# Performance work log

Measured on AMD Instinct MI355X. Metric: run time of the kernel, lower is better.

The kernel has to match this reference:

```python
import jax, jax.numpy as jnp
import numpy as np

B, DIN, DOUT = 16, 64, 64
P1_, P2_, P3_ = 64, 32, 16
BN_EPS = 1e-5


def setup_inputs() -> dict:
    key = jax.random.key(0)
    ks = jax.random.split(key, 8)
    A = jax.random.normal(ks[0], (B, DIN, P1_, P2_, P3_), dtype=jnp.float32)
    ini_p = float(np.sqrt(3.0 / DOUT / DIN))
    ini_qk = float(np.sqrt(1.0 / DOUT / DIN))
    def uni(k, s):
        return jax.random.uniform(k, (DOUT, DIN), dtype=jnp.float32, minval=-s, maxval=s)
    return {
        "A": A,
        "P1": uni(ks[1], ini_p),
        "P2": uni(ks[2], ini_p),
        "P3": uni(ks[3], ini_p),
        "P4": uni(ks[4], ini_p),
        "q": uni(ks[5], ini_qk),
        "k": uni(ks[6], ini_qk),
        "gamma": jnp.ones((DOUT,), jnp.float32),
        "beta": jnp.zeros((DOUT,), jnp.float32),
        "permutation_size1": P1_,
        "permutation_size2": P2_,
        "permutation_size3": P3_,
        "BATCH_SIZE": B,
    }


def reference(A, P1, P2, P3, P4, q, k, gamma, beta,
              permutation_size1, permutation_size2, permutation_size3, BATCH_SIZE):
    b = BATCH_SIZE
    dout = P1.shape[0]
    p1, p2, p3 = permutation_size1, permutation_size2, permutation_size3
    # branch 1: full per-element channel mix  [B, dout, p1, p2, p3]
    A1 = jnp.einsum('oi,bixyz->boxyz', P1, A)
    # branch 2: mean over p3, project, broadcast over p3
    A2 = jnp.einsum('oi,bixy->boxy', P2, A.mean(-1))[..., None]
    # branch 3: mean over p2, project, broadcast over p2
    A3 = jnp.einsum('oi,bixz->boxz', P3, A.mean(-2))[:, :, :, None, :]
    # attention over p1 with flattened (p2*p3) as the contraction axis
    Q = jnp.einsum('oi,bixyz->boxyz', q, A).reshape(b, dout, p1, p2 * p3)
    K = jnp.einsum('oi,bixyz->boxyz', k, A).reshape(b, dout, p1, p2 * p3)
    Alpha = jnp.einsum('bcxm,bcym->bcxy', Q, K)  # [B, dout, p1, p1]
    Alpha_norm = jnp.abs(Alpha) / jnp.linalg.norm(Alpha, axis=3, keepdims=True)
    V = jnp.einsum('oi,bixyz->boxyz', P4, A).reshape(b, dout, p1, p2 * p3)
    Y = jnp.einsum('bcxy,bcym->bcxm', Alpha_norm, V).reshape(b, dout, p1, p2, p3)
    out = A1 + 0.1 * A2 + 0.1 * A3 + 0.1 * Y
    out = jax.nn.relu(out)
    # BatchNorm3d (training-mode batch statistics, biased variance)
    mean = out.mean(axis=(0, 2, 3, 4), keepdims=True)
    var = out.var(axis=(0, 2, 3, 4), keepdims=True)
    out = (out - mean) * jax.lax.rsqrt(var + BN_EPS)
    out = out * gamma[None, :, None, None, None] + beta[None, :, None, None, None]
    return out
```

## Files before the change

### kernel.cpp

```cpp
#include <hip/hip_runtime.h>

typedef __attribute__((ext_vector_type(8))) short short8;
typedef __attribute__((ext_vector_type(4))) float f32x4;
typedef __attribute__((ext_vector_type(8))) unsigned short u16x8;
typedef __attribute__((ext_vector_type(4))) unsigned short u16x4;
typedef __attribute__((ext_vector_type(4))) unsigned int u32x4;
typedef unsigned short u16;

#define DEVINL __device__ __forceinline__

DEVINL u16 f2bf(float f) {
  unsigned u = __builtin_bit_cast(unsigned, f);
  unsigned r = (u + 0x7fffu + ((u >> 16) & 1u)) >> 16;
  return (u16)r;
}
DEVINL float bf2f(u16 h) {
  unsigned u = ((unsigned)h) << 16;
  return __builtin_bit_cast(float, u);
}
DEVINL unsigned pk2(float a, float b) {
  return (unsigned)f2bf(a) | ((unsigned)f2bf(b) << 16);
}
DEVINL int swzc(int row, int chunk) { return chunk ^ ((row ^ (row >> 3)) & 7); }
DEVINL int tile_byte(int row, int chunk) { return row * 128 + swzc(row, chunk) * 16; }

__global__ void kw_convert(const float* __restrict__ P1, const float* __restrict__ q,
                           const float* __restrict__ k, const float* __restrict__ P4,
                           const float* __restrict__ P2, const float* __restrict__ P3,
                           u16* __restrict__ Wbf) {
  int t = threadIdx.x;
  const float* srcs[6] = {P1, q, k, P4, P2, P3};
  for (int w = 0; w < 6; ++w)
    for (int e = t; e < 4096; e += 256) Wbf[w * 4096 + e] = f2bf(srcs[w][e]);
}

__global__ __launch_bounds__(512) void k_projA(
    const float* __restrict__ A, const u16* __restrict__ Wbf, u16* __restrict__ A1,
    u16* __restrict__ Q, u16* __restrict__ Km, u16* __restrict__ V,
    float* __restrict__ A2g, float* __restrict__ m2p, int g0) {
  __shared__ __align__(16) u16 tile[256 * 64];
  __shared__ __align__(16) u16 meanT[16 * 64];
  const int t = threadIdx.x;
  const int w = t >> 6, l = t & 63;
  const int lr = l & 15, lh = l >> 4;
  const int T = blockIdx.x, bg = blockIdx.y;
  const int x = T >> 1, h = T & 1;
  const long bglob = g0 + bg;

  const int m = w & 3, sh = w >> 2;
  const u16* wb = Wbf + m * 4096;
  short8 wf[4][2];
#pragma unroll
  for (int ot = 0; ot < 4; ++ot)
#pragma unroll
    for (int ks = 0; ks < 2; ++ks)
      wf[ot][ks] = *(const short8*)(wb + (ot * 16 + lr) * 64 + ks * 32 + lh * 8);
  u16* outp = (m == 0) ? A1 : (m == 1) ? Q : (m == 2) ? Km : V;
  outp += (long)bg * 64 * 32768;
  const int odd = lh & 1;
  const int p8 = (lh >> 1) * 8;

  {
    const int s4 = t & 31, i4 = t >> 5;
    const float* ap =
        A + (bglob * 64 + i4 * 4) * 32768 + (long)x * 512 + h * 256 + s4 * 4;
#pragma unroll
    for (int si = 0; si < 2; ++si) {
      f32x4 v0 = *(const f32x4*)(ap + si * 128);
      f32x4 v1 = *(const f32x4*)(ap + si * 128 + 32768);
      f32x4 v2 = *(const f32x4*)(ap + si * 128 + 65536);
      f32x4 v3 = *(const f32x4*)(ap + si * 128 + 98304);
#pragma unroll
      for (int e = 0; e < 4; ++e) {
        int s = si * 128 + s4 * 4 + e;
        u16x4 pk = {f2bf(v0[e]), f2bf(v1[e]), f2bf(v2[e]), f2bf(v3[e])};
        *(u16x4*)((char*)tile + tile_byte(s, i4 >> 1) + (i4 & 1) * 8) = pk;
      }
    }
  }
  __syncthreads();

  {
    const int ic = t & 7, zq = (t >> 3) & 3, y16 = t >> 5;
    float acc[8] = {0, 0, 0, 0, 0, 0, 0, 0};
#pragma unroll
    for (int zz = 0; zz < 4; ++zz) {
      int row = y16 * 16 + zq * 4 + zz;
      u16x8 v = *(const u16x8*)((const char*)tile + tile_byte(row, ic));
#pragma unroll
      for (int e = 0; e < 8; ++e) acc[e] += bf2f(v[e]);
    }
#pragma unroll
    for (int e = 0; e < 8; ++e) {
      acc[e] += __shfl_xor(acc[e], 8);
      acc[e] += __shfl_xor(acc[e], 16);
    }
    if (zq == 0) {
      u16x8 pk;
#pragma unroll
      for (int e = 0; e < 8; ++e) pk[e] = f2bf(acc[e] * (1.0f / 16.0f));
      *(u16x8*)((char*)meanT + tile_byte(y16, ic)) = pk;
    }
  }
  {
    const int ic = t & 7, yg = (t >> 3) & 3, z = t >> 5;
    float acc[8] = {0, 0, 0, 0, 0, 0, 0, 0};
#pragma unroll
    for (int yy = 0; yy < 4; ++yy) {
      int row = (yg * 4 + yy) * 16 + z;
      u16x8 v = *(const u16x8*)((const char*)tile + tile_byte(row, ic));
#pragma unroll
      for (int e = 0; e < 8; ++e) acc[e] += bf2f(v[e]);
    }
#pragma unroll
    for (int e = 0; e < 8; ++e) {
      acc[e] += __shfl_xor(acc[e], 8);
      acc[e] += __shfl_xor(acc[e], 16);
    }
    if (yg == 0) {
      float* mp = m2p + (((long)bg * 64 + x) * 2 + h) * 1024 + z * 64 + ic * 8;
      *(f32x4*)(mp) = (f32x4){acc[0], acc[1], acc[2], acc[3]};
      *(f32x4*)(mp + 4) = (f32x4){acc[4], acc[5], acc[6], acc[7]};
    }
  }

  for (int stp = 0; stp < 4; ++stp) {
    const int srowE = sh * 128 + stp * 32 + lr;
    const int srowO = srowE + 16;
    short8 aE0 = *(const short8*)((const char*)tile + tile_byte(srowE, lh));
    short8 aE1 = *(const short8*)((const char*)tile + tile_byte(srowE, 4 + lh));
    short8 aO0 = *(const short8*)((const char*)tile + tile_byte(srowO, lh));
    short8 aO1 = *(const short8*)((const char*)tile + tile_byte(srowO, 4 + lh));
    const int sbase = x * 512 + h * 256 + sh * 128 + stp * 32 + odd * 16 + p8;
#pragma unroll
    for (int ot = 0; ot < 4; ++ot) {
      f32x4 accE = {0.0f, 0.0f, 0.0f, 0.0f}, accO = {0.0f, 0.0f, 0.0f, 0.0f};
      accE = __builtin_amdgcn_mfma_f32_16x16x32_bf16(aE0, wf[ot][0], accE, 0, 0, 0);
      accE = __builtin_amdgcn_mfma_f32_16x16x32_bf16(aE1, wf[ot][1], accE, 0, 0, 0);
      accO = __builtin_amdgcn_mfma_f32_16x16x32_bf16(aO0, wf[ot][0], accO, 0, 0, 0);
      accO = __builtin_amdgcn_mfma_f32_16x16x32_bf16(aO1, wf[ot][1], accO, 0, 0, 0);
      unsigned pE0 = pk2(accE[0], accE[1]), pE1 = pk2(accE[2], accE[3]);
      unsigned pO0 = pk2(accO[0], accO[1]), pO1 = pk2(accO[2], accO[3]);
      unsigned rE0 = __shfl_xor((int)pE0, 16), rE1 = __shfl_xor((int)pE1, 16);
      unsigned rO0 = __shfl_xor((int)pO0, 16), rO1 = __shfl_xor((int)pO1, 16);
      u32x4 sv;
      if (odd) sv = (u32x4){rO0, rO1, pO0, pO1};
      else     sv = (u32x4){pE0, pE1, rE0, rE1};
      *(u32x4*)(outp + (long)(ot * 16 + lr) * 32768 + sbase) = sv;
    }
  }
  __syncthreads();

  if (w == 0) {
    const u16* wb2 = Wbf + 4 * 4096;
    f32x4 acc2[4];
#pragma unroll
    for (int ot = 0; ot < 4; ++ot) acc2[ot] = {0.0f, 0.0f, 0.0f, 0.0f};
#pragma unroll
    for (int ks = 0; ks < 2; ++ks) {
      short8 mf = *(const short8*)((const char*)meanT + tile_byte(lr, ks * 4 + lh));
#pragma unroll
      for (int ot = 0; ot < 4; ++ot) {
        short8 w2f = *(const short8*)(wb2 + (ot * 16 + lr) * 64 + ks * 32 + lh * 8);
        acc2[ot] = __builtin_amdgcn_mfma_f32_16x16x32_bf16(w2f, mf, acc2[ot], 0, 0, 0);
      }
    }
#pragma unroll
    for (int ot = 0; ot < 4; ++ot)
#pragma unroll
      for (int r = 0; r < 4; ++r) {
        int o = ot * 16 + lh * 4 + r;
        A2g[(((long)bg * 64 + o) * 64 + x) * 32 + h * 16 + lr] = acc2[ot][r];
      }
  }
}

__global__ __launch_bounds__(256) void k_a3fin(const float* __restrict__ m2p,
                                               const float* __restrict__ P3,
                                               float* __restrict__ A3g, int g0) {
  __shared__ float m2s[16 * 65];
  const int t = threadIdx.x;
  const int x = blockIdx.x, bg = blockIdx.y;
  const float* mp = m2p + ((long)bg * 64 + x) * 2048;
  {
    int e = t * 4;
    int z = e >> 6, i = e & 63;
    f32x4 v0 = *(const f32x4*)(mp + e);
    f32x4 v1 = *(const f32x4*)(mp + 1024 + e);
#pragma unroll
    for (int j = 0; j < 4; ++j) m2s[z * 65 + i + j] = (v0[j] + v1[j]) * (1.0f / 32.0f);
  }
  __syncthreads();
  const int z = t & 15, og = t >> 4;
#pragma unroll
  for (int oo = 0; oo < 4; ++oo) {
    int o = og * 4 + oo;
    float acc = 0.0f;
#pragma unroll 8
    for (int i = 0; i < 64; ++i) acc += P3[o * 64 + i] * m2s[z * 65 + i];
    A3g[(((long)bg * 64 + o) * 64 + x) * 16 + z] = acc;
  }
}

__global__ __launch_bounds__(256) void k_attn(const u16* __restrict__ Qg,
                                              const u16* __restrict__ Kg,
                                              const u16* __restrict__ Vg,
                                              const u16* __restrict__ A1g,
                                              const float* __restrict__ A2g,
                                              const float* __restrict__ A3g,
                                              u16* __restrict__ outbf,
                                              float* __restrict__ partials, int g0) {
  __shared__ __align__(16) u16 Qc[4096], Kc[4096];
  __shared__ __align__(16) u16 Vt[2][4096];
  __shared__ __align__(16) u16 An[4096];
  __shared__ float red[8];
  const int t = threadIdx.x, w = t >> 6, l = t & 63;
  const int lr = l & 15, lh = l >> 4;
  const int c = blockIdx.x, bg = blockIdx.y;
  const long bglob = g0 + bg;
  const long base = ((long)bg * 64 + c) * 32768;
  const u16* Qp = Qg + base;
  const u16* Kp = Kg + base;
  const u16* Vp = Vg + base;
  const u16* A1p = A1g + base;

  const int m4 = t & 15, y4 = t >> 4;
  const int odd = lh & 1;
  const int p8 = (lh >> 1) * 8;

  u16x4 vr[4];
#pragma unroll
  for (int r = 0; r < 4; ++r)
    vr[r] = *(const u16x4*)(Vp + (y4 * 4 + r) * 512 + m4 * 4);

  f32x4 accA[4];
#pragma unroll
  for (int yt = 0; yt < 4; ++yt) accA[yt] = {0.0f, 0.0f, 0.0f, 0.0f};

  const int srow = t >> 3, scc = t & 7;
  u16x8 qpre[2], kpre[2];
#pragma unroll
  for (int it = 0; it < 2; ++it) {
    int row = srow + it * 32;
    int gch = scc ^ ((row ^ (row >> 3)) & 7);
    qpre[it] = *(const u16x8*)(Qp + row * 512 + gch * 8);
    kpre[it] = *(const u16x8*)(Kp + row * 512 + gch * 8);
  }
  for (int mc = 0; mc < 8; ++mc) {
#pragma unroll
    for (int it = 0; it < 2; ++it) {
      int row = srow + it * 32;
      *(u16x8*)((char*)Qc + row * 128 + scc * 16) = qpre[it];
      *(u16x8*)((char*)Kc + row * 128 + scc * 16) = kpre[it];
    }
    asm volatile("s_waitcnt lgkmcnt(0)" ::: "memory");
    __builtin_amdgcn_s_barrier();
    __builtin_amdgcn_sched_barrier(0);
    if (mc < 7) {
      const int nc = (mc + 1) * 64;
#pragma unroll
      for (int it = 0; it < 2; ++it) {
        int row = srow + it * 32;
        int gch = scc ^ ((row ^ (row >> 3)) & 7);
        qpre[it] = *(const u16x8*)(Qp + row * 512 + nc + gch * 8);
        kpre[it] = *(const u16x8*)(Kp + row * 512 + nc + gch * 8);
      }
    }
    short8 qf[2];
#pragma unroll
    for (int ks = 0; ks < 2; ++ks)
      qf[ks] = *(const short8*)((const char*)Qc + tile_byte(16 * w + lr, ks * 4 + lh));
#pragma unroll
    for (int ks = 0; ks < 2; ++ks)
#pragma unroll
      for (int yt = 0; yt < 4; ++yt) {
        short8 kf = *(const short8*)((const char*)Kc + tile_byte(yt * 16 + lr, ks * 4 + lh));
        accA[yt] = __builtin_amdgcn_mfma_f32_16x16x32_bf16(qf[ks], kf, accA[yt], 0, 0, 0);
      }
    asm volatile("s_waitcnt lgkmcnt(0)" ::: "memory");
    __builtin_amdgcn_s_barrier();
    __builtin_amdgcn_sched_barrier(0);
  }

  float rsq[4];
#pragma unroll
  for (int r = 0; r < 4; ++r) {
    float s = 0.0f;
#pragma unroll
    for (int yt = 0; yt < 4; ++yt) s += accA[yt][r] * accA[yt][r];
#pragma unroll
    for (int msk = 1; msk < 16; msk <<= 1) s += __shfl_xor(s, msk);
    rsq[r] = rsqrtf(s);
  }
#pragma unroll
  for (int yt = 0; yt < 4; ++yt)
#pragma unroll
    for (int r = 0; r < 4; ++r) {
      int xr = 16 * w + 4 * lh + r;
      int y = yt * 16 + lr;
      *(u16*)((char*)An + xr * 128 + swzc(xr, y >> 3) * 16 + (y & 7) * 2) =
          f2bf(fabsf(accA[yt][r]) * rsq[r]);
    }

  float ls = 0.0f, lsq = 0.0f;
  const float* A2p = A2g + ((long)bg * 64 + c) * 2048;
  const float* A3p = A3g + ((long)bg * 64 + c) * 1024;
  u16* outp = outbf + (bglob * 64 + c) * 32768;
  const int x = 16 * w + lr;
  const f32x4 a3lo = *(const f32x4*)(A3p + x * 16 + p8);
  const f32x4 a3hi = *(const f32x4*)(A3p + x * 16 + p8 + 4);

  for (int mc = 0; mc < 8; ++mc) {
    u16* vbuf = Vt[mc & 1];
#pragma unroll
    for (int ci = 0; ci < 4; ++ci) {
      int mrow = m4 * 4 + ci;
      u16x4 pk = {vr[0][ci], vr[1][ci], vr[2][ci], vr[3][ci]};
      *(u16x4*)((char*)vbuf + tile_byte(mrow, y4 >> 1) + (y4 & 1) * 8) = pk;
    }
    asm volatile("s_waitcnt lgkmcnt(0)" ::: "memory");
    __builtin_amdgcn_s_barrier();
    __builtin_amdgcn_sched_barrier(0);
    if (mc < 7) {
      const int nc = (mc + 1) * 64;
#pragma unroll
      for (int r = 0; r < 4; ++r)
        vr[r] = *(const u16x4*)(Vp + (y4 * 4 + r) * 512 + nc + m4 * 4);
    }

    f32x4 accY[4];
#pragma unroll
    for (int mt = 0; mt < 4; ++mt) accY[mt] = {0.0f, 0.0f, 0.0f, 0.0f};
#pragma unroll
    for (int ks = 0; ks < 2; ++ks) {
      short8 anf = *(const short8*)((const char*)An + tile_byte(16 * w + lr, ks * 4 + lh));
#pragma unroll
      for (int mt = 0; mt < 4; ++mt) {
        short8 vf = *(const short8*)((const char*)vbuf + tile_byte(mt * 16 + lr, ks * 4 + lh));
        accY[mt] = __builtin_amdgcn_mfma_f32_16x16x32_bf16(vf, anf, accY[mt], 0, 0, 0);
      }
    }
#pragma unroll
    for (int pair = 0; pair < 2; ++pair) {
      f32x4 aE = accY[2 * pair], aO = accY[2 * pair + 1];
      f32x4 rE, rO;
#pragma unroll
      for (int j = 0; j < 4; ++j) {
        rE[j] = __shfl_xor(aE[j], 16);
        rO[j] = __shfl_xor(aO[j], 16);
      }
      const int mb = mc * 64 + pair * 32 + odd * 16 + p8;
      const float a2v = A2p[x * 32 + (mb >> 4)];
      u16x8 a1v = *(const u16x8*)(A1p + x * 512 + mb);
      u16x8 o;
#pragma unroll
      for (int r = 0; r < 8; ++r) {
        float yv = (r < 4) ? (odd ? rO[r] : aE[r]) : (odd ? aO[r - 4] : rE[r - 4]);
        float a3v = (r < 4) ? a3lo[r] : a3hi[r - 4];
        float val = bf2f(a1v[r]) + 0.1f * (a2v + a3v + yv);
        val = fmaxf(val, 0.0f);
        o[r] = f2bf(val);
        ls += val;
        lsq += val * val;
      }
      *(u16x8*)(outp + x * 512 + mb) = o;
    }
  }

#pragma unroll
  for (int off = 32; off > 0; off >>= 1) {
    ls += __shfl_xor(ls, off);
    lsq += __shfl_xor(lsq, off);
  }
  if (l == 0) {
    red[w] = ls;
    red[4 + w] = lsq;
  }
  __syncthreads();
  if (t == 0) {
    partials[2 * (bglob * 64 + c) + 0] = red[0] + red[1] + red[2] + red[3];
    partials[2 * (bglob * 64 + c) + 1] = red[4] + red[5] + red[6] + red[7];
  }
}

__global__ void k_stats(const float* __restrict__ partials, const float* __restrict__ gamma,
                        const float* __restrict__ beta, float* __restrict__ sb) {
  int c = threadIdx.x;
  if (c >= 64) return;
  float S = 0.0f, SQ = 0.0f;
  for (int b = 0; b < 16; ++b) {
    S += partials[2 * (b * 64 + c) + 0];
    SQ += partials[2 * (b * 64 + c) + 1];
  }
  const float N = 524288.0f;
  float mean = S / N;
  float var = SQ / N - mean * mean;
  float rs = rsqrtf(var + 1e-5f);
  float scale = gamma[c] * rs;
  sb[c] = scale;
  sb[64 + c] = beta[c] - mean * scale;
}

__global__ void k_bn(const u16* __restrict__ outbf, float* __restrict__ out,
                     const float* __restrict__ sb) {
  long idx = ((long)blockIdx.x * 256 + threadIdx.x) * 8;
  int c = (int)((idx >> 15) & 63);
  float scale = sb[c], bias = sb[64 + c];
  u16x8 v = *(const u16x8*)(outbf + idx);
  f32x4 o0, o1;
#pragma unroll
  for (int r = 0; r < 4; ++r) {
    o0[r] = bf2f(v[r]) * scale + bias;
    o1[r] = bf2f(v[4 + r]) * scale + bias;
  }
  *(f32x4*)(out + idx) = o0;
  *(f32x4*)(out + idx + 4) = o1;
}

extern "C" void kernel_launch(void* const* d_in, const int* in_sizes, int n_in, void* d_out,
                              int out_size, void* d_ws, size_t ws_size, hipStream_t stream) {
  (void)in_sizes; (void)n_in; (void)out_size;
  const float* A = (const float*)d_in[0];
  const float* P1 = (const float*)d_in[1];
  const float* P2 = (const float*)d_in[2];
  const float* P3 = (const float*)d_in[3];
  const float* P4 = (const float*)d_in[4];
  const float* q = (const float*)d_in[5];
  const float* k = (const float*)d_in[6];
  const float* gamma = (const float*)d_in[7];
  const float* beta = (const float*)d_in[8];
  float* out = (float*)d_out;
  char* ws = (char*)d_ws;

  u16* Wbf = (u16*)ws;
  float* partials = (float*)(ws + 49152);
  float* sb = (float*)(ws + 57344);
  const size_t GR = 65536;
  const size_t OUTBF = (size_t)16 * 64 * 32768 * 2;
  u16* outbf = (u16*)(ws + GR);
  const size_t SZ_M = (size_t)64 * 32768 * 2;
  const size_t SZ_A2 = (size_t)64 * 64 * 32 * 4;
  const size_t SZ_A3 = (size_t)64 * 64 * 16 * 4;
  const size_t SZ_M2 = (size_t)64 * 2 * 16 * 64 * 4;
  const size_t perb = 4 * SZ_M + SZ_A2 + SZ_A3 + SZ_M2;
  const size_t base0 = GR + OUTBF;
  int G = 1;
  if (ws_size > base0 + perb) G = (int)((ws_size - base0) / perb);
  if (G > 8) G = 8;
  if (G < 1) G = 1;

  u16* A1 = (u16*)(ws + base0);
  u16* Qw = (u16*)(ws + base0 + (size_t)G * SZ_M);
  u16* Kw = (u16*)(ws + base0 + (size_t)G * SZ_M * 2);
  u16* Vw = (u16*)(ws + base0 + (size_t)G * SZ_M * 3);
  float* A2 = (float*)(ws + base0 + (size_t)G * SZ_M * 4);
  float* A3 = (float*)((char*)A2 + (size_t)G * SZ_A2);
  float* m2p = (float*)((char*)A3 + (size_t)G * SZ_A3);

  kw_convert<<<1, 256, 0, stream>>>(P1, q, k, P4, P2, P3, Wbf);
  for (int g0 = 0; g0 < 16; g0 += G) {
    int Gc = (16 - g0) < G ? (16 - g0) : G;
    k_projA<<<dim3(128, Gc), 512, 0, stream>>>(A, Wbf, A1, Qw, Kw, Vw, A2, m2p, g0);
    k_a3fin<<<dim3(64, Gc), 256, 0, stream>>>(m2p, P3, A3, g0);
    k_attn<<<dim3(64, Gc), 256, 0, stream>>>(Qw, Kw, Vw, A1, A2, A3, outbf, partials, g0);
  }
  k_stats<<<1, 64, 0, stream>>>(partials, gamma, beta, sb);
  k_bn<<<16384, 256, 0, stream>>>(outbf, out, sb);
}
```

Measured before the change: 243.6 us.

## Store intermediates in x-major layout so projection writes are contiguous per block

The intermediate Q/K/V/A1 and the pre-BN output buffers switch from channel-major [b][c][x][m] to x-major [b][x][c][m]. Each projection block (one x position) then writes a contiguous 64x512 slab instead of 64 strided 1KB rows, and the attention kernel instead reads with a 64KB stride per row. The BN kernel is rewritten so each block transposes one (b,x) slab back to the channel-major fp32 output. This trades write locality in k_projA for strided reads in k_attn and a transpose in k_bn.

```diff
diff --git a/kernel.cpp b/kernel.cpp
--- a/kernel.cpp
+++ b/kernel.cpp
@@ -23,6 +23,7 @@
 }
 DEVINL int swzc(int row, int chunk) { return chunk ^ ((row ^ (row >> 3)) & 7); }
 DEVINL int tile_byte(int row, int chunk) { return row * 128 + swzc(row, chunk) * 16; }
+
 
 __global__ void kw_convert(const float* __restrict__ P1, const float* __restrict__ q,
                            const float* __restrict__ k, const float* __restrict__ P4,
@@ -56,7 +57,7 @@
     for (int ks = 0; ks < 2; ++ks)
       wf[ot][ks] = *(const short8*)(wb + (ot * 16 + lr) * 64 + ks * 32 + lh * 8);
   u16* outp = (m == 0) ? A1 : (m == 1) ? Q : (m == 2) ? Km : V;
-  outp += (long)bg * 64 * 32768;
+  outp += ((long)bg * 64 + x) * 32768;
   const int odd = lh & 1;
   const int p8 = (lh >> 1) * 8;
 
@@ -131,7 +132,7 @@
     short8 aE1 = *(const short8*)((const char*)tile + tile_byte(srowE, 4 + lh));
     short8 aO0 = *(const short8*)((const char*)tile + tile_byte(srowO, lh));
     short8 aO1 = *(const short8*)((const char*)tile + tile_byte(srowO, 4 + lh));
-    const int sbase = x * 512 + h * 256 + sh * 128 + stp * 32 + odd * 16 + p8;
+    const int mloc = h * 256 + sh * 128 + stp * 32 + odd * 16 + p8;
 #pragma unroll
     for (int ot = 0; ot < 4; ++ot) {
       f32x4 accE = {0.0f, 0.0f, 0.0f, 0.0f}, accO = {0.0f, 0.0f, 0.0f, 0.0f};
@@ -146,7 +147,7 @@
       u32x4 sv;
       if (odd) sv = (u32x4){rO0, rO1, pO0, pO1};
       else     sv = (u32x4){pE0, pE1, rE0, rE1};
-      *(u32x4*)(outp + (long)(ot * 16 + lr) * 32768 + sbase) = sv;
+      *(u32x4*)(outp + (ot * 16 + lr) * 512 + mloc) = sv;
     }
   }
   __syncthreads();
@@ -218,7 +219,7 @@
   const int lr = l & 15, lh = l >> 4;
   const int c = blockIdx.x, bg = blockIdx.y;
   const long bglob = g0 + bg;
-  const long base = ((long)bg * 64 + c) * 32768;
+  const long base = (long)bg * 2097152 + (long)c * 512;
   const u16* Qp = Qg + base;
   const u16* Kp = Kg + base;
   const u16* Vp = Vg + base;
@@ -231,7 +232,7 @@
   u16x4 vr[4];
 #pragma unroll
   for (int r = 0; r < 4; ++r)
-    vr[r] = *(const u16x4*)(Vp + (y4 * 4 + r) * 512 + m4 * 4);
+    vr[r] = *(const u16x4*)(Vp + (long)(y4 * 4 + r) * 32768 + m4 * 4);
 
   f32x4 accA[4];
 #pragma unroll
@@ -243,8 +244,8 @@
   for (int it = 0; it < 2; ++it) {
     int row = srow + it * 32;
     int gch = scc ^ ((row ^ (row >> 3)) & 7);
-    qpre[it] = *(const u16x8*)(Qp + row * 512 + gch * 8);
-    kpre[it] = *(const u16x8*)(Kp + row * 512 + gch * 8);
+    qpre[it] = *(const u16x8*)(Qp + (long)row * 32768 + gch * 8);
+    kpre[it] = *(const u16x8*)(Kp + (long)row * 32768 + gch * 8);
   }
   for (int mc = 0; mc < 8; ++mc) {
 #pragma unroll
@@ -262,8 +263,8 @@
       for (int it = 0; it < 2; ++it) {
         int row = srow + it * 32;
         int gch = scc ^ ((row ^ (row >> 3)) & 7);
-        qpre[it] = *(const u16x8*)(Qp + row * 512 + nc + gch * 8);
-        kpre[it] = *(const u16x8*)(Kp + row * 512 + nc + gch * 8);
+        qpre[it] = *(const u16x8*)(Qp + (long)row * 32768 + nc + gch * 8);
+        kpre[it] = *(const u16x8*)(Kp + (long)row * 32768 + nc + gch * 8);
       }
     }
     short8 qf[2];
@@ -305,7 +306,7 @@
   float ls = 0.0f, lsq = 0.0f;
   const float* A2p = A2g + ((long)bg * 64 + c) * 2048;
   const float* A3p = A3g + ((long)bg * 64 + c) * 1024;
-  u16* outp = outbf + (bglob * 64 + c) * 32768;
+  u16* outp = outbf + (long)bglob * 2097152 + (long)c * 512;
   const int x = 16 * w + lr;
   const f32x4 a3lo = *(const f32x4*)(A3p + x * 16 + p8);
   const f32x4 a3hi = *(const f32x4*)(A3p + x * 16 + p8 + 4);
@@ -325,7 +326,7 @@
       const int nc = (mc + 1) * 64;
 #pragma unroll
       for (int r = 0; r < 4; ++r)
-        vr[r] = *(const u16x4*)(Vp + (y4 * 4 + r) * 512 + nc + m4 * 4);
+        vr[r] = *(const u16x4*)(Vp + (long)(y4 * 4 + r) * 32768 + nc + m4 * 4);
     }
 
     f32x4 accY[4];
@@ -351,7 +352,7 @@
       }
       const int mb = mc * 64 + pair * 32 + odd * 16 + p8;
       const float a2v = A2p[x * 32 + (mb >> 4)];
-      u16x8 a1v = *(const u16x8*)(A1p + x * 512 + mb);
+      u16x8 a1v = *(const u16x8*)(A1p + (long)x * 32768 + mb);
       u16x8 o;
 #pragma unroll
       for (int r = 0; r < 8; ++r) {
@@ -363,7 +364,7 @@
         ls += val;
         lsq += val * val;
       }
-      *(u16x8*)(outp + x * 512 + mb) = o;
+      *(u16x8*)(outp + (long)x * 32768 + mb) = o;
     }
   }
 
@@ -401,20 +402,28 @@
   sb[64 + c] = beta[c] - mean * scale;
 }
 
-__global__ void k_bn(const u16* __restrict__ outbf, float* __restrict__ out,
-                     const float* __restrict__ sb) {
-  long idx = ((long)blockIdx.x * 256 + threadIdx.x) * 8;
-  int c = (int)((idx >> 15) & 63);
-  float scale = sb[c], bias = sb[64 + c];
-  u16x8 v = *(const u16x8*)(outbf + idx);
-  f32x4 o0, o1;
-#pragma unroll
-  for (int r = 0; r < 4; ++r) {
-    o0[r] = bf2f(v[r]) * scale + bias;
-    o1[r] = bf2f(v[4 + r]) * scale + bias;
-  }
-  *(f32x4*)(out + idx) = o0;
-  *(f32x4*)(out + idx + 4) = o1;
+__global__ __launch_bounds__(256) void k_bn(const u16* __restrict__ outbf,
+                                            float* __restrict__ out,
+                                            const float* __restrict__ sb) {
+  const int x = blockIdx.x & 63, b = blockIdx.x >> 6;
+  const u16* tin = outbf + ((long)b * 64 + x) * 32768;
+  float* outb = out + (long)b * 2097152 + (long)x * 512;
+#pragma unroll
+  for (int rep = 0; rep < 16; ++rep) {
+    int e = rep * 2048 + threadIdx.x * 8;
+    int cc = e >> 9, mm = e & 511;
+    u16x8 v = *(const u16x8*)(tin + e);
+    float scale = sb[cc], bias = sb[64 + cc];
+    f32x4 o0, o1;
+#pragma unroll
+    for (int r = 0; r < 4; ++r) {
+      o0[r] = bf2f(v[r]) * scale + bias;
+      o1[r] = bf2f(v[4 + r]) * scale + bias;
+    }
+    float* op = outb + (long)cc * 32768 + mm;
+    *(f32x4*)(op) = o0;
+    *(f32x4*)(op + 4) = o1;
+  }
 }
 
 extern "C" void kernel_launch(void* const* d_in, const int* in_sizes, int n_in, void* d_out,
@@ -465,5 +474,5 @@
     k_attn<<<dim3(64, Gc), 256, 0, stream>>>(Qw, Kw, Vw, A1, A2, A3, outbf, partials, g0);
   }
   k_stats<<<1, 64, 0, stream>>>(partials, gamma, beta, sb);
-  k_bn<<<16384, 256, 0, stream>>>(outbf, out, sb);
-}
+  k_bn<<<1024, 256, 0, stream>>>(outbf, out, sb);
+}
```

After: 247.1 us. No clear change (+1.4%).
